# Kernel tuning notes

Measured on AMD Instinct MI355X. Metric: run time of the kernel, lower is better.

The kernel has to match this reference:

```python
import jax, jax.numpy as jnp
import numpy as np

K = 3  # kernel_size
PAD = 1


def _unfold3x3(x):
    # x: [b, c, h, w] -> patches [b, c, k*k, h, w] matching torch.nn.Unfold
    # ordering (row-major over the kernel window, channel outermost).
    b, c, h, w = x.shape
    xp = jnp.pad(x, ((0, 0), (0, 0), (PAD, PAD), (PAD, PAD)))
    patches = jnp.stack(
        [xp[:, :, i:i + h, j:j + w] for i in range(K) for j in range(K)],
        axis=2,
    )
    return patches  # [b, c, 9, h, w]


def setup_inputs() -> dict:
    key = jax.random.key(0)
    k1, k2, k3, k4 = jax.random.split(key, 4)
    b, c, h, w = 8, 64, 128, 128
    out_ch = 64
    x = jax.random.normal(k1, (b, c, h, w), dtype=jnp.float32)
    guide_ch = jax.random.normal(k2, (b, c, h, w), dtype=jnp.float32)
    guide_sp = jax.random.normal(k3, (b, K * K, h, w), dtype=jnp.float32)
    # kaiming_normal_ fan_out on [out, in, k^2, 1, 1]: fan_out = out * k^2 * 1 * 1?
    # torch fan_out for 5D conv weight = out_channels * receptive_field (k^2*1*1)
    fan_out = out_ch * (K * K)
    std = np.sqrt(2.0 / fan_out)
    weight = jax.random.normal(k4, (out_ch, c, K * K), dtype=jnp.float32) * std
    return {"x": x, "guide_ch": guide_ch, "guide_sp": guide_sp, "weight": weight}


def reference(x, guide_ch, guide_sp, weight):
    # filter: [b, c, k^2, h, w] = 1 + tanh(guide_ch[:, :, None] + guide_sp[:, None])
    filt = 1.0 + jnp.tanh(guide_ch[:, :, None, :, :] + guide_sp[:, None, :, :, :])
    patches = _unfold3x3(x)  # [b, c, 9, h, w]
    # conv3d with weight [out, in, k^2, 1, 1] == per-pixel reduction over (c, k^2)
    out = jnp.einsum('bckhw,ock->bohw', patches * filt, weight)
    return out
```

## Files before the change

kernel.cpp:

```cpp
#include <hip/hip_runtime.h>
#include <hip/hip_bf16.h>

typedef short short8 __attribute__((ext_vector_type(8)));
typedef float floatx4 __attribute__((ext_vector_type(4)));
typedef unsigned uintx4 __attribute__((ext_vector_type(4)));

#define HWSZ 16384
#define WD 128
#define CD 64
#define OD 64
#define XSTR 72
#define OSTR 136
#define L2E2 2.8853900817779268f

__device__ __forceinline__ short f2bf(float f) {
    unsigned u = __builtin_bit_cast(unsigned, f);
    u += 0x7FFFu + ((u >> 16) & 1u);
    return (short)(u >> 16);
}

__device__ __forceinline__ unsigned pack2bf(float a, float b) {
    __hip_bfloat162 h = __float22bfloat162_rn(float2{a, b});
    unsigned u;
    __builtin_memcpy(&u, &h, 4);
    return u;
}

__device__ __forceinline__ float bf2f(short s) {
    return __builtin_bit_cast(float, ((unsigned)(unsigned short)s) << 16);
}

__global__ void prepack_w(const float* __restrict__ wgt, unsigned short* __restrict__ wp) {
    int idx = blockIdx.x * 256 + threadIdx.x;
    if (idx < 9 * 64 * 64) {
        int k = idx >> 12, o = (idx >> 6) & 63, c = idx & 63;
        wp[idx] = (unsigned short)f2bf(2.0f * wgt[o * 576 + c * 9 + k]);
    }
}

__global__ __launch_bounds__(256, 3)
void paka_kernel(const float* __restrict__ x, const float* __restrict__ gc,
                 const float* __restrict__ gs, const float* __restrict__ wgt,
                 const unsigned short* __restrict__ wp, float* __restrict__ out)
{
    __shared__ union {
        struct {
            short xl[130 * XSTR];
            short wl[3][64 * XSTR];
        } s;
        float o[64 * OSTR];
    } lds;

    const int tid  = threadIdx.x;
    const int wave = tid >> 6;
    const int lane = tid & 63;
    const int b = blockIdx.x >> 7;
    const int h = blockIdx.x & 127;

    const float* xb  = x  + (size_t)b * CD * HWSZ;
    const float* gcb = gc + (size_t)b * CD * HWSZ;
    const float* gsb = gs + (size_t)b * 9 * HWSZ;

    const int row = lane & 15;
    const int q   = lane >> 4;
    const int mt0 = wave * 2;

    float eg[2][2][8];
    #pragma unroll
    for (int mt = 0; mt < 2; ++mt) {
        int p = (mt0 + mt) * 16 + row;
        #pragma unroll
        for (int ks = 0; ks < 2; ++ks)
            #pragma unroll
            for (int j = 0; j < 8; ++j) {
                int c = ks * 32 + q * 8 + j;
                eg[mt][ks][j] = __builtin_amdgcn_exp2f(gcb[(size_t)c * HWSZ + h * WD + p] * L2E2);
            }
    }
    float esv[9][2];
    #pragma unroll
    for (int k = 0; k < 9; ++k)
        #pragma unroll
        for (int mt = 0; mt < 2; ++mt) {
            int p = (mt0 + mt) * 16 + row;
            esv[k][mt] = __builtin_amdgcn_exp2f(gsb[k * HWSZ + h * WD + p] * L2E2);
        }

    if (tid < 32)
        *(unsigned*)&lds.s.xl[0 * XSTR + tid * 2] = 0u;
    else if (tid < 64)
        *(unsigned*)&lds.s.xl[129 * XSTR + (tid - 32) * 2] = 0u;

    floatx4 acc[2][4];
    #pragma unroll
    for (int i = 0; i < 2; ++i)
        #pragma unroll
        for (int n = 0; n < 4; ++n)
            acc[i][n] = (floatx4){0.f, 0.f, 0.f, 0.f};

    #pragma unroll
    for (int dh = 0; dh < 3; ++dh) {
        const int hh = h + dh - 1;
        if ((unsigned)hh >= 128u) continue;

        __syncthreads();

        if (wp) {
            #pragma unroll
            for (int it = 0; it < 6; ++it) {
                int idx = it * 256 + tid;
                int dw = idx >> 9, o = (idx >> 3) & 63, cg = idx & 7;
                short8 v = *(const short8*)&wp[(dh * 3 + dw) * 4096 + o * 64 + cg * 8];
                *(short8*)&lds.s.wl[dw][o * XSTR + cg * 8] = v;
            }
        } else {
            #pragma unroll
            for (int it = 0; it < 48; ++it) {
                int idx = it * 256 + tid;
                int dw = idx >> 12, o = (idx >> 6) & 63, c = idx & 63;
                lds.s.wl[dw][o * XSTR + c] = f2bf(2.0f * wgt[o * 576 + c * 9 + dh * 3 + dw]);
            }
        }

        {
            const int g = tid >> 5;
            const float* xg = xb + (size_t)(8 * g) * HWSZ + hh * WD;
            #pragma unroll
            for (int it = 0; it < 4; ++it) {
                int p = it * 32 + (tid & 31);
                uintx4 pv;
                #pragma unroll
                for (int cc = 0; cc < 4; ++cc) {
                    float a  = xg[(size_t)(2 * cc) * HWSZ + p];
                    float b2 = xg[(size_t)(2 * cc + 1) * HWSZ + p];
                    pv[cc] = pack2bf(a, b2);
                }
                *(uintx4*)&lds.s.xl[(p + 1) * XSTR + g * 8] = pv;
            }
        }

        __syncthreads();

        #pragma unroll
        for (int dw = 0; dw < 3; ++dw) {
            const int k = dh * 3 + dw;
            #pragma unroll
            for (int ks = 0; ks < 2; ++ks) {
                short8 af[2];
                #pragma unroll
                for (int mt = 0; mt < 2; ++mt) {
                    int wslot = (mt0 + mt) * 16 + row + dw;
                    short8 raw = *(const short8*)&lds.s.xl[wslot * XSTR + ks * 32 + q * 8];
                    float es = esv[k][mt];
                    #pragma unroll
                    for (int jj = 0; jj < 4; ++jj) {
                        float d0 = fmaf(eg[mt][ks][2 * jj],     es, 1.0f);
                        float d1 = fmaf(eg[mt][ks][2 * jj + 1], es, 1.0f);
                        float r0 = __builtin_amdgcn_rcpf(d0);
                        float r1 = __builtin_amdgcn_rcpf(d1);
                        float x0 = bf2f(raw[2 * jj]);
                        float x1 = bf2f(raw[2 * jj + 1]);
                        float t0 = fmaf(-x0, r0, x0);
                        float t1 = fmaf(-x1, r1, x1);
                        ((unsigned*)&af[mt])[jj] = pack2bf(t0, t1);
                    }
                }
                #pragma unroll
                for (int nt = 0; nt < 4; ++nt) {
                    short8 bv = *(const short8*)&lds.s.wl[dw][(nt * 16 + row) * XSTR + ks * 32 + q * 8];
                    acc[0][nt] = __builtin_amdgcn_mfma_f32_16x16x32_bf16(af[0], bv, acc[0][nt], 0, 0, 0);
                    acc[1][nt] = __builtin_amdgcn_mfma_f32_16x16x32_bf16(af[1], bv, acc[1][nt], 0, 0, 0);
                }
            }
        }
    }

    __syncthreads();

    #pragma unroll
    for (int i = 0; i < 2; ++i) {
        int prow = (mt0 + i) * 16 + q * 4;
        #pragma unroll
        for (int nt = 0; nt < 4; ++nt) {
            int o = nt * 16 + row;
            *(floatx4*)&lds.o[o * OSTR + prow] = acc[i][nt];
        }
    }

    __syncthreads();

    float* outb = out + ((size_t)b * OD) * HWSZ + h * WD;
    #pragma unroll
    for (int it = 0; it < 8; ++it) {
        int idx = it * 256 + tid;
        int o = idx >> 5, p4 = (idx & 31) * 4;
        *(floatx4*)&outb[(size_t)o * HWSZ + p4] = *(const floatx4*)&lds.o[o * OSTR + p4];
    }
}

extern "C" void kernel_launch(void* const* d_in, const int* in_sizes, int n_in,
                              void* d_out, int out_size, void* d_ws, size_t ws_size,
                              hipStream_t stream) {
    const float* x   = (const float*)d_in[0];
    const float* gcp = (const float*)d_in[1];
    const float* gsp = (const float*)d_in[2];
    const float* wgt = (const float*)d_in[3];
    float* out = (float*)d_out;

    const bool use_wp = ws_size >= (size_t)(9 * 64 * 64 * sizeof(unsigned short));
    unsigned short* wp = use_wp ? (unsigned short*)d_ws : nullptr;
    if (use_wp)
        prepack_w<<<dim3(144), dim3(256), 0, stream>>>(wgt, wp);
    paka_kernel<<<dim3(1024), dim3(256), 0, stream>>>(x, gcp, gsp, wgt, wp, out);
}
```

Before: 139.7 us.

## Double-buffer input rows in LDS, read weights from global, swizzle block order

New measurement: 189.3 us. +35.5%, slower.

```diff
diff --git a/kernel.cpp b/kernel.cpp
--- a/kernel.cpp
+++ b/kernel.cpp
@@ -38,24 +38,53 @@
     }
 }
 
+__device__ __forceinline__ void load_row(const float* __restrict__ xg, bool zero,
+                                         int tid, uintx4 pv[4]) {
+    if (!zero) {
+        #pragma unroll
+        for (int it = 0; it < 4; ++it) {
+            int p = it * 32 + (tid & 31);
+            #pragma unroll
+            for (int cc = 0; cc < 4; ++cc) {
+                float a  = xg[(size_t)(2 * cc) * HWSZ + p];
+                float b2 = xg[(size_t)(2 * cc + 1) * HWSZ + p];
+                pv[it][cc] = pack2bf(a, b2);
+            }
+        }
+    } else {
+        #pragma unroll
+        for (int it = 0; it < 4; ++it) pv[it] = (uintx4){0u, 0u, 0u, 0u};
+    }
+}
+
+__device__ __forceinline__ void store_row(short* __restrict__ xbuf,
+                                          const uintx4 pv[4], int tid) {
+    const int g = tid >> 5;
+    #pragma unroll
+    for (int it = 0; it < 4; ++it) {
+        int p = it * 32 + (tid & 31);
+        *(uintx4*)&xbuf[(p + 1) * XSTR + g * 8] = pv[it];
+    }
+}
+
 __global__ __launch_bounds__(256, 3)
 void paka_kernel(const float* __restrict__ x, const float* __restrict__ gc,
                  const float* __restrict__ gs, const float* __restrict__ wgt,
                  const unsigned short* __restrict__ wp, float* __restrict__ out)
 {
     __shared__ union {
-        struct {
-            short xl[130 * XSTR];
-            short wl[3][64 * XSTR];
-        } s;
+        short xb2[2][130 * XSTR];
         float o[64 * OSTR];
     } lds;
 
     const int tid  = threadIdx.x;
     const int wave = tid >> 6;
     const int lane = tid & 63;
-    const int b = blockIdx.x >> 7;
-    const int h = blockIdx.x & 127;
+
+    const int id  = blockIdx.x;
+    const int swz = (id & 7) * 128 + (id >> 3);
+    const int b = swz >> 7;
+    const int h = swz & 127;
 
     const float* xb  = x  + (size_t)b * CD * HWSZ;
     const float* gcb = gc + (size_t)b * CD * HWSZ;
@@ -64,6 +93,7 @@
     const int row = lane & 15;
     const int q   = lane >> 4;
     const int mt0 = wave * 2;
+    const int g   = tid >> 5;
 
     float eg[2][2][8];
     #pragma unroll
@@ -86,10 +116,14 @@
             esv[k][mt] = __builtin_amdgcn_exp2f(gsb[k * HWSZ + h * WD + p] * L2E2);
         }
 
-    if (tid < 32)
-        *(unsigned*)&lds.s.xl[0 * XSTR + tid * 2] = 0u;
-    else if (tid < 64)
-        *(unsigned*)&lds.s.xl[129 * XSTR + (tid - 32) * 2] = 0u;
+    if (tid < 32) {
+        *(unsigned*)&lds.xb2[0][0 * XSTR + tid * 2] = 0u;
+        *(unsigned*)&lds.xb2[1][0 * XSTR + tid * 2] = 0u;
+    } else if (tid < 64) {
+        int t = tid - 32;
+        *(unsigned*)&lds.xb2[0][129 * XSTR + t * 2] = 0u;
+        *(unsigned*)&lds.xb2[1][129 * XSTR + t * 2] = 0u;
+    }
 
     floatx4 acc[2][4];
     #pragma unroll
@@ -98,59 +132,49 @@
         for (int n = 0; n < 4; ++n)
             acc[i][n] = (floatx4){0.f, 0.f, 0.f, 0.f};
 
+    const float* xg0 = xb + (size_t)(8 * g) * HWSZ;
+    uintx4 pv[4];
+
+    load_row(xg0 + (size_t)(h - 1) * WD, h == 0, tid, pv);
+    store_row(lds.xb2[0], pv, tid);
+    load_row(xg0 + (size_t)h * WD, false, tid, pv);
+    __syncthreads();
+
     #pragma unroll
     for (int dh = 0; dh < 3; ++dh) {
-        const int hh = h + dh - 1;
-        if ((unsigned)hh >= 128u) continue;
-
-        __syncthreads();
-
-        if (wp) {
-            #pragma unroll
-            for (int it = 0; it < 6; ++it) {
-                int idx = it * 256 + tid;
-                int dw = idx >> 9, o = (idx >> 3) & 63, cg = idx & 7;
-                short8 v = *(const short8*)&wp[(dh * 3 + dw) * 4096 + o * 64 + cg * 8];
-                *(short8*)&lds.s.wl[dw][o * XSTR + cg * 8] = v;
-            }
-        } else {
-            #pragma unroll
-            for (int it = 0; it < 48; ++it) {
-                int idx = it * 256 + tid;
-                int dw = idx >> 12, o = (idx >> 6) & 63, c = idx & 63;
-                lds.s.wl[dw][o * XSTR + c] = f2bf(2.0f * wgt[o * 576 + c * 9 + dh * 3 + dw]);
-            }
-        }
-
-        {
-            const int g = tid >> 5;
-            const float* xg = xb + (size_t)(8 * g) * HWSZ + hh * WD;
-            #pragma unroll
-            for (int it = 0; it < 4; ++it) {
-                int p = it * 32 + (tid & 31);
-                uintx4 pv;
-                #pragma unroll
-                for (int cc = 0; cc < 4; ++cc) {
-                    float a  = xg[(size_t)(2 * cc) * HWSZ + p];
-                    float b2 = xg[(size_t)(2 * cc + 1) * HWSZ + p];
-                    pv[cc] = pack2bf(a, b2);
-                }
-                *(uintx4*)&lds.s.xl[(p + 1) * XSTR + g * 8] = pv;
-            }
-        }
-
-        __syncthreads();
+        if (dh < 2)
+            store_row(lds.xb2[(dh + 1) & 1], pv, tid);
+        if (dh == 0)
+            load_row(xg0 + (size_t)(h + 1) * WD, h == 127, tid, pv);
+
+        const short* rbuf = lds.xb2[dh & 1];
 
         #pragma unroll
         for (int dw = 0; dw < 3; ++dw) {
             const int k = dh * 3 + dw;
             #pragma unroll
             for (int ks = 0; ks < 2; ++ks) {
+                short8 bv[4];
+                if (wp) {
+                    const unsigned short* wk = wp + k * 4096 + ks * 32 + q * 8;
+                    #pragma unroll
+                    for (int nt = 0; nt < 4; ++nt)
+                        bv[nt] = *(const short8*)&wk[(nt * 16 + row) * 64];
+                } else {
+                    #pragma unroll
+                    for (int nt = 0; nt < 4; ++nt)
+                        #pragma unroll
+                        for (int j = 0; j < 8; ++j) {
+                            int o = nt * 16 + row, c = ks * 32 + q * 8 + j;
+                            bv[nt][j] = f2bf(2.0f * wgt[o * 576 + c * 9 + k]);
+                        }
+                }
+
                 short8 af[2];
                 #pragma unroll
                 for (int mt = 0; mt < 2; ++mt) {
                     int wslot = (mt0 + mt) * 16 + row + dw;
-                    short8 raw = *(const short8*)&lds.s.xl[wslot * XSTR + ks * 32 + q * 8];
+                    short8 raw = *(const short8*)&rbuf[wslot * XSTR + ks * 32 + q * 8];
                     float es = esv[k][mt];
                     #pragma unroll
                     for (int jj = 0; jj < 4; ++jj) {
@@ -167,15 +191,13 @@
                 }
                 #pragma unroll
                 for (int nt = 0; nt < 4; ++nt) {
-                    short8 bv = *(const short8*)&lds.s.wl[dw][(nt * 16 + row) * XSTR + ks * 32 + q * 8];
-                    acc[0][nt] = __builtin_amdgcn_mfma_f32_16x16x32_bf16(af[0], bv, acc[0][nt], 0, 0, 0);
-                    acc[1][nt] = __builtin_amdgcn_mfma_f32_16x16x32_bf16(af[1], bv, acc[1][nt], 0, 0, 0);
+                    acc[0][nt] = __builtin_amdgcn_mfma_f32_16x16x32_bf16(af[0], bv[nt], acc[0][nt], 0, 0, 0);
+                    acc[1][nt] = __builtin_amdgcn_mfma_f32_16x16x32_bf16(af[1], bv[nt], acc[1][nt], 0, 0, 0);
                 }
             }
         }
-    }
-
-    __syncthreads();
+        __syncthreads();
+    }
 
     #pragma unroll
     for (int i = 0; i < 2; ++i) {
```

## Read weights from global/L2 directly, shrink LDS, raise occupancy, swizzle blocks

Applied to the files above, without the earlier changes.

Measured after the change: 222.0 us. 1.59x slower.

```diff
diff --git a/kernel.cpp b/kernel.cpp
--- a/kernel.cpp
+++ b/kernel.cpp
@@ -38,24 +38,24 @@
     }
 }
 
-__global__ __launch_bounds__(256, 3)
+__global__ __launch_bounds__(256, 4)
 void paka_kernel(const float* __restrict__ x, const float* __restrict__ gc,
                  const float* __restrict__ gs, const float* __restrict__ wgt,
                  const unsigned short* __restrict__ wp, float* __restrict__ out)
 {
     __shared__ union {
-        struct {
-            short xl[130 * XSTR];
-            short wl[3][64 * XSTR];
-        } s;
+        short xl[130 * XSTR];
         float o[64 * OSTR];
     } lds;
 
     const int tid  = threadIdx.x;
     const int wave = tid >> 6;
     const int lane = tid & 63;
-    const int b = blockIdx.x >> 7;
-    const int h = blockIdx.x & 127;
+
+    const int id  = blockIdx.x;
+    const int swz = (id & 7) * 128 + (id >> 3);
+    const int b = swz >> 7;
+    const int h = swz & 127;
 
     const float* xb  = x  + (size_t)b * CD * HWSZ;
     const float* gcb = gc + (size_t)b * CD * HWSZ;
@@ -87,9 +87,9 @@
         }
 
     if (tid < 32)
-        *(unsigned*)&lds.s.xl[0 * XSTR + tid * 2] = 0u;
+        *(unsigned*)&lds.xl[0 * XSTR + tid * 2] = 0u;
     else if (tid < 64)
-        *(unsigned*)&lds.s.xl[129 * XSTR + (tid - 32) * 2] = 0u;
+        *(unsigned*)&lds.xl[129 * XSTR + (tid - 32) * 2] = 0u;
 
     floatx4 acc[2][4];
     #pragma unroll
@@ -104,23 +104,6 @@
         if ((unsigned)hh >= 128u) continue;
 
         __syncthreads();
-
-        if (wp) {
-            #pragma unroll
-            for (int it = 0; it < 6; ++it) {
-                int idx = it * 256 + tid;
-                int dw = idx >> 9, o = (idx >> 3) & 63, cg = idx & 7;
-                short8 v = *(const short8*)&wp[(dh * 3 + dw) * 4096 + o * 64 + cg * 8];
-                *(short8*)&lds.s.wl[dw][o * XSTR + cg * 8] = v;
-            }
-        } else {
-            #pragma unroll
-            for (int it = 0; it < 48; ++it) {
-                int idx = it * 256 + tid;
-                int dw = idx >> 12, o = (idx >> 6) & 63, c = idx & 63;
-                lds.s.wl[dw][o * XSTR + c] = f2bf(2.0f * wgt[o * 576 + c * 9 + dh * 3 + dw]);
-            }
-        }
 
         {
             const int g = tid >> 5;
@@ -135,7 +118,7 @@
                     float b2 = xg[(size_t)(2 * cc + 1) * HWSZ + p];
                     pv[cc] = pack2bf(a, b2);
                 }
-                *(uintx4*)&lds.s.xl[(p + 1) * XSTR + g * 8] = pv;
+                *(uintx4*)&lds.xl[(p + 1) * XSTR + g * 8] = pv;
             }
         }
 
@@ -146,11 +129,27 @@
             const int k = dh * 3 + dw;
             #pragma unroll
             for (int ks = 0; ks < 2; ++ks) {
+                short8 bv[4];
+                if (wp) {
+                    const unsigned short* wk = wp + k * 4096 + ks * 32 + q * 8;
+                    #pragma unroll
+                    for (int nt = 0; nt < 4; ++nt)
+                        bv[nt] = *(const short8*)&wk[(nt * 16 + row) * 64];
+                } else {
+                    #pragma unroll
+                    for (int nt = 0; nt < 4; ++nt)
+                        #pragma unroll
+                        for (int j = 0; j < 8; ++j) {
+                            int o = nt * 16 + row, c = ks * 32 + q * 8 + j;
+                            bv[nt][j] = f2bf(2.0f * wgt[o * 576 + c * 9 + k]);
+                        }
+                }
+
                 short8 af[2];
                 #pragma unroll
                 for (int mt = 0; mt < 2; ++mt) {
                     int wslot = (mt0 + mt) * 16 + row + dw;
-                    short8 raw = *(const short8*)&lds.s.xl[wslot * XSTR + ks * 32 + q * 8];
+                    short8 raw = *(const short8*)&lds.xl[wslot * XSTR + ks * 32 + q * 8];
                     float es = esv[k][mt];
                     #pragma unroll
                     for (int jj = 0; jj < 4; ++jj) {
@@ -167,9 +166,8 @@
                 }
                 #pragma unroll
                 for (int nt = 0; nt < 4; ++nt) {
-                    short8 bv = *(const short8*)&lds.s.wl[dw][(nt * 16 + row) * XSTR + ks * 32 + q * 8];
-                    acc[0][nt] = __builtin_amdgcn_mfma_f32_16x16x32_bf16(af[0], bv, acc[0][nt], 0, 0, 0);
-                    acc[1][nt] = __builtin_amdgcn_mfma_f32_16x16x32_bf16(af[1], bv, acc[1][nt], 0, 0, 0);
+                    acc[0][nt] = __builtin_amdgcn_mfma_f32_16x16x32_bf16(af[0], bv[nt], acc[0][nt], 0, 0, 0);
+                    acc[1][nt] = __builtin_amdgcn_mfma_f32_16x16x32_bf16(af[1], bv[nt], acc[1][nt], 0, 0, 0);
                 }
             }
         }
```
